# Optimization experiments

Hardware: AMD Instinct MI355X
Metric: run time of the kernel (lower is better)

Reference implementation:

```python
import jax, jax.numpy as jnp
import numpy as np

B, T, E, H = 8, 2048, 512, 16
D = E // H  # 32 embeddings per head
LN_EPS = 1e-3  # keras LayerNormalization default epsilon
DECAY = 1.2


def setup_inputs() -> dict:
    key = jax.random.key(0)
    k0, k1, k2 = jax.random.split(key, 3)
    x = jax.random.normal(k0, (B, T, E), dtype=jnp.float32)
    W = jax.random.normal(k1, (E, E), dtype=jnp.float32) * (1.0 / np.sqrt(E))
    b = jnp.zeros((E,), dtype=jnp.float32)
    concept_map = jax.random.normal(k2, (H, D, D, D), dtype=jnp.float32) * 0.02
    gamma = jnp.ones((E,), dtype=jnp.float32)
    beta = jnp.zeros((E,), dtype=jnp.float32)
    return {"x": x, "W": W, "b": b, "concept_map": concept_map,
            "gamma": gamma, "beta": beta}


def reference(x, W, b, concept_map, gamma, beta):
    Bn, Tn, En = x.shape
    Hn = concept_map.shape[0]
    Dn = En // Hn
    # Dense projection, split into heads: (B,T,H,D)
    h = (jnp.einsum('bte,ef->btf', x, W) + b).reshape(Bn, Tn, Hn, Dn)
    # Decayed cumulative sum of preceding tokens: S_0 = 0, S_t = (S_{t-1} + h_{t-1}) / 1.2
    def step(s, h_t):
        return (s + h_t) / DECAY, s
    _, S = jax.lax.scan(step, jnp.zeros((Bn, Hn, Dn), h.dtype),
                        jnp.swapaxes(h, 0, 1))  # S: (T,B,H,D)
    S = jnp.swapaxes(S, 0, 1)  # (B,T,H,D)
    # Fused bilinear contraction: sum_{i,j} h[...,i] * S[...,j] * C[h,k,i,j]
    # (equivalent to outer-product * concept_map then reduce_sum over last two dims)
    y = jnp.einsum('bthi,bthj,hkij->bthk', h, S, concept_map) + h
    y = y.reshape(Bn, Tn, En)
    # LayerNormalization over last axis (keras default eps=1e-3)
    mu = jnp.mean(y, axis=-1, keepdims=True)
    var = jnp.var(y, axis=-1, keepdims=True)
    y = (y - mu) * jax.lax.rsqrt(var + LN_EPS) * gamma + beta
    # Dropout: identity at inference
    return y
```

## Files before the change

### kernel.cpp

```cpp
#include <hip/hip_runtime.h>
#include <hip/hip_bf16.h>

#define Bn 8
#define Tn 2048
#define En 512
#define Hn 16
#define Dn 32
#define NC 32
#define CL 64
#define NT (Bn*Tn)
#define INV_DECAY (1.0f/1.2f)

typedef __attribute__((ext_vector_type(8))) short  bf16x8;
typedef __attribute__((ext_vector_type(8))) _Float16 f16x8;
typedef __attribute__((ext_vector_type(2))) _Float16 f16x2;
typedef __attribute__((ext_vector_type(4))) float  f32x4;
typedef __attribute__((ext_vector_type(8))) unsigned short u16x8;

__device__ __forceinline__ unsigned short f2b(float f) {
    __hip_bfloat16 h = __float2bfloat16(f);
    return *reinterpret_cast<unsigned short*>(&h);
}
__device__ __forceinline__ float b2f(unsigned short u) {
    union { unsigned int i; float f; } c; c.i = ((unsigned int)u) << 16; return c.f;
}
__device__ __forceinline__ unsigned short f2h(float f) {
    union { _Float16 h; unsigned short u; } c; c.h = (_Float16)f; return c.u;
}

__host__ __device__ constexpr float wpow(int e) {
    float r = 1.f;
    for (int i = 0; i < e; i++) r *= (1.0f / 1.2f);
    return r;
}

__device__ __forceinline__ size_t hm(int hd, int tok, int ch) {
    return (size_t)hd * ((size_t)NT * Dn) + (size_t)tok * Dn + ch;
}

__global__ __launch_bounds__(256) void prep_k(const float* __restrict__ C,
                                              unsigned short* __restrict__ Cl,
                                              const float* __restrict__ W,
                                              unsigned short* __restrict__ Wt) {
    __shared__ float tile[32][33];
    if (blockIdx.x < 256) {
        const int g = blockIdx.x * 256 + threadIdx.x;
        const int hd = g >> 12, rem = g & 4095;
        const int i = rem >> 7, half = (rem >> 6) & 1, lane = rem & 63;
        const int tloc = lane & 15, kgrp = lane >> 4;
        const int k = half * 16 + tloc;
        const float* src = C + (size_t)hd * 32768 + (size_t)k * 1024 + i * 32 + kgrp * 8;
        float4 a = reinterpret_cast<const float4*>(src)[0];
        float4 b = reinterpret_cast<const float4*>(src)[1];
        u16x8 st;
        st[0]=f2h(a.x); st[1]=f2h(a.y); st[2]=f2h(a.z); st[3]=f2h(a.w);
        st[4]=f2h(b.x); st[5]=f2h(b.y); st[6]=f2h(b.z); st[7]=f2h(b.w);
        *reinterpret_cast<u16x8*>(Cl + (size_t)g * 8) = st;
    } else {
        const int bid = blockIdx.x - 256;
        const int kb = (bid & 15) * 32, nb = (bid >> 4) * 32;
        const int tx = threadIdx.x & 31, ty = threadIdx.x >> 5;
        #pragma unroll
        for (int j = 0; j < 4; j++)
            tile[ty + 8 * j][tx] = W[(size_t)(kb + ty + 8 * j) * En + nb + tx];
        __syncthreads();
        #pragma unroll
        for (int j = 0; j < 4; j++)
            Wt[(size_t)(nb + ty + 8 * j) * En + kb + tx] = f2b(tile[tx][ty + 8 * j]);
    }
}

__global__ __launch_bounds__(256) void gemm_mfma_k(const float* __restrict__ x,
                                                   const unsigned short* __restrict__ Wt,
                                                   const float* __restrict__ bias,
                                                   unsigned short* __restrict__ h,
                                                   float* __restrict__ locals) {
    __shared__ unsigned short As[128][40];
    __shared__ unsigned short Bs[64][40];
    const int m0 = blockIdx.x * 128, n0 = blockIdx.y * 64;
    const int tid = threadIdx.x;
    const int wid = tid >> 6, lane = tid & 63;
    const int tloc = lane & 15, kgrp = lane >> 4;
    const int wr = wid >> 1, wc = wid & 1;

    const int ar = tid >> 1, ah = (tid & 1) * 16;
    const int brr = tid >> 2, bq = (tid & 3) * 8;

    f32x4 acc[4][2] = {};

    for (int k0 = 0; k0 < En; k0 += 32) {
        const float* xp = &x[(size_t)(m0 + ar) * En + k0 + ah];
        float4 a0 = reinterpret_cast<const float4*>(xp)[0];
        float4 a1 = reinterpret_cast<const float4*>(xp)[1];
        float4 a2 = reinterpret_cast<const float4*>(xp)[2];
        float4 a3 = reinterpret_cast<const float4*>(xp)[3];
        u16x8 bv = *reinterpret_cast<const u16x8*>(&Wt[(size_t)(n0 + brr) * En + k0 + bq]);
        __syncthreads();
        u16x8 w0, w1;
        w0[0]=f2b(a0.x); w0[1]=f2b(a0.y); w0[2]=f2b(a0.z); w0[3]=f2b(a0.w);
        w0[4]=f2b(a1.x); w0[5]=f2b(a1.y); w0[6]=f2b(a1.z); w0[7]=f2b(a1.w);
        w1[0]=f2b(a2.x); w1[1]=f2b(a2.y); w1[2]=f2b(a2.z); w1[3]=f2b(a2.w);
        w1[4]=f2b(a3.x); w1[5]=f2b(a3.y); w1[6]=f2b(a3.z); w1[7]=f2b(a3.w);
        *reinterpret_cast<u16x8*>(&As[ar][ah])     = w0;
        *reinterpret_cast<u16x8*>(&As[ar][ah + 8]) = w1;
        *reinterpret_cast<u16x8*>(&Bs[brr][bq])    = bv;
        __syncthreads();

        bf16x8 afr[4], bfr[2];
        #pragma unroll
        for (int m = 0; m < 4; m++)
            afr[m] = *reinterpret_cast<const bf16x8*>(&As[wr * 64 + m * 16 + tloc][kgrp * 8]);
        #pragma unroll
        for (int n = 0; n < 2; n++)
            bfr[n] = *reinterpret_cast<const bf16x8*>(&Bs[wc * 32 + n * 16 + tloc][kgrp * 8]);
        #pragma unroll
        for (int m = 0; m < 4; m++)
            #pragma unroll
            for (int n = 0; n < 2; n++)
                acc[m][n] = __builtin_amdgcn_mfma_f32_16x16x32_bf16(afr[m], bfr[n], acc[m][n], 0, 0, 0);
    }

    const float kmul = (kgrp & 1 ? 2.0736f : 1.f) * (kgrp & 2 ? 4.29981696f : 1.f);
    const int cg = blockIdx.x * 2 + wr;

    #pragma unroll
    for (int n = 0; n < 2; n++) {
        const int col = n0 + wc * 32 + n * 16 + tloc;
        const float bcol = bias[col];
        const int hd = col >> 5, ch = col & 31;
        float part = 0.f;
        #pragma unroll
        for (int m = 0; m < 4; m++)
            #pragma unroll
            for (int r = 0; r < 4; r++) {
                const int row = m0 + wr * 64 + m * 16 + kgrp * 4 + r;
                const unsigned short hb16 = f2b(acc[m][n][r] + bcol);
                h[hm(hd, row, ch)] = hb16;
                part += b2f(hb16) * (wpow(64 - m * 16 - r) * kmul);
            }
        part += __shfl_xor(part, 16);
        part += __shfl_xor(part, 32);
        if (kgrp == 0) locals[(size_t)cg * En + col] = part;
    }
}

__global__ __launch_bounds__(512) void scan_emit3_k(const unsigned short* __restrict__ h,
                                                    const float* __restrict__ locals,
                                                    unsigned short* __restrict__ Sg) {
    const int c = blockIdx.x, b = blockIdx.y;
    const int e = threadIdx.x;
    const int hd = e >> 5, ch = e & 31;
    constexpr float INVRL = wpow(64);

    float A = 0.f, w = 1.f;
    for (int cp = c - 1; cp >= 0; --cp) {
        A += w * locals[(size_t)(b * NC + cp) * En + e];
        w *= INVRL;
    }

    const size_t base = hm(hd, b * Tn + c * CL, ch);
    for (int t = 0; t < CL; t++) {
        Sg[base + (size_t)t * Dn] = f2h(A);
        A = (A + b2f(h[base + (size_t)t * Dn])) * INV_DECAY;
    }
}

__global__ __launch_bounds__(256, 4) void bilinear14_k(const unsigned short* __restrict__ hg,
                                                       const unsigned short* __restrict__ Sg,
                                                       unsigned short* __restrict__ yb,
                                                       const unsigned short* __restrict__ Cl) {
    __shared__ float ys[4][64][36];

    const int hd = blockIdx.y;
    const int tid = threadIdx.x;
    const int wid = tid >> 6, lane = tid & 63;
    const int tloc = lane & 15, kgrp = lane >> 4;
    const int j0 = kgrp * 8;
    const int tokens0 = blockIdx.x * 64;

    f16x8 afr[8][2];
    {
        const unsigned short* cb = Cl + (size_t)hd * 32768;
        #pragma unroll
        for (int s = 0; s < 8; s++) {
            const int i = wid * 8 + s;
            #pragma unroll
            for (int mt = 0; mt < 2; mt++)
                afr[s][mt] = *reinterpret_cast<const f16x8*>(
                    cb + ((size_t)((i * 2 + mt) * 64 + lane) * 8));
        }
    }

    _Float16 hh[4][8];
    f16x2 sf2[4][4];
    #pragma unroll
    for (int nt = 0; nt < 4; nt++) {
        const int trow = tokens0 + nt * 16 + tloc;
        u16x8 hv = *reinterpret_cast<const u16x8*>(hg + hm(hd, trow, wid * 8));
        #pragma unroll
        for (int e = 0; e < 8; e++) hh[nt][e] = (_Float16)b2f(hv[e]);
        f16x8 svh = *reinterpret_cast<const f16x8*>(Sg + hm(hd, trow, j0));
        #pragma unroll
        for (int e2 = 0; e2 < 4; e2++) {
            f16x2 p; p.x = svh[e2 * 2]; p.y = svh[e2 * 2 + 1];
            sf2[nt][e2] = p;
        }
    }

    f32x4 acc[2][4] = {};
    #pragma unroll
    for (int s = 0; s < 8; s++) {
        #pragma unroll
        for (int nt = 0; nt < 4; nt++) {
            f16x2 hb; hb.x = hh[nt][s]; hb.y = hh[nt][s];
            union { f16x8 v; f16x2 p[4]; } bf;
            bf.p[0] = sf2[nt][0] * hb;
            bf.p[1] = sf2[nt][1] * hb;
            bf.p[2] = sf2[nt][2] * hb;
            bf.p[3] = sf2[nt][3] * hb;
            acc[0][nt] = __builtin_amdgcn_mfma_f32_16x16x32_f16(afr[s][0], bf.v, acc[0][nt], 0, 0, 0);
            acc[1][nt] = __builtin_amdgcn_mfma_f32_16x16x32_f16(afr[s][1], bf.v, acc[1][nt], 0, 0, 0);
        }
    }

    #pragma unroll
    for (int mt = 0; mt < 2; mt++)
        #pragma unroll
        for (int nt = 0; nt < 4; nt++)
            *reinterpret_cast<f32x4*>(&ys[wid][nt * 16 + tloc][mt * 16 + kgrp * 4]) = acc[mt][nt];
    __syncthreads();

    {
        const int token = tid >> 2, q = tid & 3;
        f32x4 y0 = {0.f,0.f,0.f,0.f}, y1 = {0.f,0.f,0.f,0.f};
        #pragma unroll
        for (int w = 0; w < 4; w++) {
            const f32x4* src = reinterpret_cast<const f32x4*>(&ys[w][token][q * 8]);
            y0 += src[0];
            y1 += src[1];
        }
        u16x8 hres = *reinterpret_cast<const u16x8*>(hg + hm(hd, tokens0 + token, q * 8));
        u16x8 st;
        #pragma unroll
        for (int e = 0; e < 4; e++) {
            st[e]     = f2b(y0[e] + b2f(hres[e]));
            st[4 + e] = f2b(y1[e] + b2f(hres[4 + e]));
        }
        *reinterpret_cast<u16x8*>(yb + hm(hd, tokens0 + token, q * 8)) = st;
    }
}

__global__ __launch_bounds__(256) void ln_k(const unsigned short* __restrict__ y,
                                            const float* __restrict__ gamma,
                                            const float* __restrict__ beta,
                                            float* __restrict__ out) {
    const int row = blockIdx.x * 4 + (threadIdx.x >> 6);
    const int lane = threadIdx.x & 63;
    u16x8 v = *reinterpret_cast<const u16x8*>(y + hm(lane >> 2, row, (lane & 3) * 8));
    float f[8];
    float s = 0.f, s2 = 0.f;
    #pragma unroll
    for (int e = 0; e < 8; e++) {
        f[e] = b2f(v[e]);
        s += f[e]; s2 += f[e] * f[e];
    }
    #pragma unroll
    for (int off = 1; off < 64; off <<= 1) {
        s  += __shfl_xor(s, off);
        s2 += __shfl_xor(s2, off);
    }
    const float mu = s * (1.f / En);
    const float var = s2 * (1.f / En) - mu * mu;
    const float rs = rsqrtf(var + 1e-3f);
    const int cbase = lane * 8;
    float4 g0 = reinterpret_cast<const float4*>(&gamma[cbase])[0];
    float4 g1 = reinterpret_cast<const float4*>(&gamma[cbase])[1];
    float4 b0 = reinterpret_cast<const float4*>(&beta[cbase])[0];
    float4 b1 = reinterpret_cast<const float4*>(&beta[cbase])[1];
    float4 o0, o1;
    o0.x = (f[0] - mu) * rs * g0.x + b0.x; o0.y = (f[1] - mu) * rs * g0.y + b0.y;
    o0.z = (f[2] - mu) * rs * g0.z + b0.z; o0.w = (f[3] - mu) * rs * g0.w + b0.w;
    o1.x = (f[4] - mu) * rs * g1.x + b1.x; o1.y = (f[5] - mu) * rs * g1.y + b1.y;
    o1.z = (f[6] - mu) * rs * g1.z + b1.z; o1.w = (f[7] - mu) * rs * g1.w + b1.w;
    float* op = out + (size_t)row * En;
    reinterpret_cast<float4*>(op)[lane * 2]     = o0;
    reinterpret_cast<float4*>(op)[lane * 2 + 1] = o1;
}

extern "C" void kernel_launch(void* const* d_in, const int* in_sizes, int n_in,
                              void* d_out, int out_size, void* d_ws, size_t ws_size,
                              hipStream_t stream) {
    const float* x     = (const float*)d_in[0];
    const float* W     = (const float*)d_in[1];
    const float* bias  = (const float*)d_in[2];
    const float* C     = (const float*)d_in[3];
    const float* gamma = (const float*)d_in[4];
    const float* beta  = (const float*)d_in[5];
    float* out = (float*)d_out;

    unsigned short* hb  = (unsigned short*)d_ws;
    unsigned short* Sg  = hb + (size_t)Hn * NT * Dn;
    unsigned short* Cl  = Sg + (size_t)Hn * NT * Dn;
    unsigned short* Wt  = Cl + (size_t)Hn * Dn * Dn * Dn;
    float* locals = (float*)(Wt + (size_t)En * En);

    prep_k<<<512, 256, 0, stream>>>(C, Cl, W, Wt);
    gemm_mfma_k<<<dim3(NT / 128, En / 64), 256, 0, stream>>>(x, Wt, bias, hb, locals);
    scan_emit3_k<<<dim3(NC, Bn), 512, 0, stream>>>(hb, locals, Sg);
    bilinear14_k<<<dim3(NT / CL, Hn), 256, 0, stream>>>(hb, Sg, Sg , Cl);
    ln_k<<<NT / 4, 256, 0, stream>>>(Sg, gamma, beta, out);
}
```

Baseline: 76.52 us.

## Switch intermediates from bf16 to fp16 and widen GEMM N-tile to 128

All intermediate tensors (W transpose, projected h, y) now use fp16 instead of bf16, so the GEMM runs fp16 MFMA and the bilinear kernel loads h directly as f16 vectors with no per-element bf16-to-f16 conversion. The projection GEMM tile grows from 128x64 to 128x128, doubling per-warp accumulators and halving the grid, so the x tile is converted and staged in LDS half as often. The costs are fp16 range and overflow risk on h and y, higher register pressure, and fewer blocks available to fill the GPU.

Result: no change. 76.55 us (median of 2 runs) (+0.0%).

```diff
diff --git a/kernel.cpp b/kernel.cpp
--- a/kernel.cpp
+++ b/kernel.cpp
@@ -11,21 +11,16 @@
 #define NT (Bn*Tn)
 #define INV_DECAY (1.0f/1.2f)
 
-typedef __attribute__((ext_vector_type(8))) short  bf16x8;
 typedef __attribute__((ext_vector_type(8))) _Float16 f16x8;
 typedef __attribute__((ext_vector_type(2))) _Float16 f16x2;
 typedef __attribute__((ext_vector_type(4))) float  f32x4;
 typedef __attribute__((ext_vector_type(8))) unsigned short u16x8;
 
-__device__ __forceinline__ unsigned short f2b(float f) {
-    __hip_bfloat16 h = __float2bfloat16(f);
-    return *reinterpret_cast<unsigned short*>(&h);
-}
-__device__ __forceinline__ float b2f(unsigned short u) {
-    union { unsigned int i; float f; } c; c.i = ((unsigned int)u) << 16; return c.f;
-}
 __device__ __forceinline__ unsigned short f2h(float f) {
     union { _Float16 h; unsigned short u; } c; c.h = (_Float16)f; return c.u;
+}
+__device__ __forceinline__ float h2f(unsigned short u) {
+    union { _Float16 h; unsigned short u; } c; c.u = u; return (float)c.h;
 }
 
 __host__ __device__ constexpr float wpow(int e) {
@@ -66,7 +61,7 @@
         __syncthreads();
         #pragma unroll
         for (int j = 0; j < 4; j++)
-            Wt[(size_t)(nb + ty + 8 * j) * En + kb + tx] = f2b(tile[tx][ty + 8 * j]);
+            Wt[(size_t)(nb + ty + 8 * j) * En + kb + tx] = f2h(tile[tx][ty + 8 * j]);
     }
 }
 
@@ -76,56 +71,58 @@
                                                    unsigned short* __restrict__ h,
                                                    float* __restrict__ locals) {
     __shared__ unsigned short As[128][40];
-    __shared__ unsigned short Bs[64][40];
-    const int m0 = blockIdx.x * 128, n0 = blockIdx.y * 64;
+    __shared__ unsigned short Bs[128][40];
+    const int m0 = blockIdx.x * 128, n0 = blockIdx.y * 128;
     const int tid = threadIdx.x;
     const int wid = tid >> 6, lane = tid & 63;
     const int tloc = lane & 15, kgrp = lane >> 4;
     const int wr = wid >> 1, wc = wid & 1;
 
-    const int ar = tid >> 1, ah = (tid & 1) * 16;
-    const int brr = tid >> 2, bq = (tid & 3) * 8;
-
-    f32x4 acc[4][2] = {};
+    const int sr = tid >> 1, sh = (tid & 1) * 16;
+
+    f32x4 acc[4][4] = {};
 
     for (int k0 = 0; k0 < En; k0 += 32) {
-        const float* xp = &x[(size_t)(m0 + ar) * En + k0 + ah];
+        const float* xp = &x[(size_t)(m0 + sr) * En + k0 + sh];
         float4 a0 = reinterpret_cast<const float4*>(xp)[0];
         float4 a1 = reinterpret_cast<const float4*>(xp)[1];
         float4 a2 = reinterpret_cast<const float4*>(xp)[2];
         float4 a3 = reinterpret_cast<const float4*>(xp)[3];
-        u16x8 bv = *reinterpret_cast<const u16x8*>(&Wt[(size_t)(n0 + brr) * En + k0 + bq]);
+        const unsigned short* wp = &Wt[(size_t)(n0 + sr) * En + k0 + sh];
+        u16x8 bv0 = reinterpret_cast<const u16x8*>(wp)[0];
+        u16x8 bv1 = reinterpret_cast<const u16x8*>(wp)[1];
         __syncthreads();
         u16x8 w0, w1;
-        w0[0]=f2b(a0.x); w0[1]=f2b(a0.y); w0[2]=f2b(a0.z); w0[3]=f2b(a0.w);
-        w0[4]=f2b(a1.x); w0[5]=f2b(a1.y); w0[6]=f2b(a1.z); w0[7]=f2b(a1.w);
-        w1[0]=f2b(a2.x); w1[1]=f2b(a2.y); w1[2]=f2b(a2.z); w1[3]=f2b(a2.w);
-        w1[4]=f2b(a3.x); w1[5]=f2b(a3.y); w1[6]=f2b(a3.z); w1[7]=f2b(a3.w);
-        *reinterpret_cast<u16x8*>(&As[ar][ah])     = w0;
-        *reinterpret_cast<u16x8*>(&As[ar][ah + 8]) = w1;
-        *reinterpret_cast<u16x8*>(&Bs[brr][bq])    = bv;
+        w0[0]=f2h(a0.x); w0[1]=f2h(a0.y); w0[2]=f2h(a0.z); w0[3]=f2h(a0.w);
+        w0[4]=f2h(a1.x); w0[5]=f2h(a1.y); w0[6]=f2h(a1.z); w0[7]=f2h(a1.w);
+        w1[0]=f2h(a2.x); w1[1]=f2h(a2.y); w1[2]=f2h(a2.z); w1[3]=f2h(a2.w);
+        w1[4]=f2h(a3.x); w1[5]=f2h(a3.y); w1[6]=f2h(a3.z); w1[7]=f2h(a3.w);
+        *reinterpret_cast<u16x8*>(&As[sr][sh])     = w0;
+        *reinterpret_cast<u16x8*>(&As[sr][sh + 8]) = w1;
+        *reinterpret_cast<u16x8*>(&Bs[sr][sh])     = bv0;
+        *reinterpret_cast<u16x8*>(&Bs[sr][sh + 8]) = bv1;
         __syncthreads();
 
-        bf16x8 afr[4], bfr[2];
+        f16x8 afr[4], bfr[4];
         #pragma unroll
         for (int m = 0; m < 4; m++)
-            afr[m] = *reinterpret_cast<const bf16x8*>(&As[wr * 64 + m * 16 + tloc][kgrp * 8]);
-        #pragma unroll
-        for (int n = 0; n < 2; n++)
-            bfr[n] = *reinterpret_cast<const bf16x8*>(&Bs[wc * 32 + n * 16 + tloc][kgrp * 8]);
+            afr[m] = *reinterpret_cast<const f16x8*>(&As[wr * 64 + m * 16 + tloc][kgrp * 8]);
+        #pragma unroll
+        for (int n = 0; n < 4; n++)
+            bfr[n] = *reinterpret_cast<const f16x8*>(&Bs[wc * 64 + n * 16 + tloc][kgrp * 8]);
         #pragma unroll
         for (int m = 0; m < 4; m++)
             #pragma unroll
-            for (int n = 0; n < 2; n++)
-                acc[m][n] = __builtin_amdgcn_mfma_f32_16x16x32_bf16(afr[m], bfr[n], acc[m][n], 0, 0, 0);
+            for (int n = 0; n < 4; n++)
+                acc[m][n] = __builtin_amdgcn_mfma_f32_16x16x32_f16(afr[m], bfr[n], acc[m][n], 0, 0, 0);
     }
 
     const float kmul = (kgrp & 1 ? 2.0736f : 1.f) * (kgrp & 2 ? 4.29981696f : 1.f);
     const int cg = blockIdx.x * 2 + wr;
 
     #pragma unroll
-    for (int n = 0; n < 2; n++) {
-        const int col = n0 + wc * 32 + n * 16 + tloc;
+    for (int nt = 0; nt < 4; nt++) {
+        const int col = n0 + wc * 64 + nt * 16 + tloc;
         const float bcol = bias[col];
         const int hd = col >> 5, ch = col & 31;
         float part = 0.f;
@@ -134,9 +131,9 @@
             #pragma unroll
             for (int r = 0; r < 4; r++) {
                 const int row = m0 + wr * 64 + m * 16 + kgrp * 4 + r;
-                const unsigned short hb16 = f2b(acc[m][n][r] + bcol);
+                const unsigned short hb16 = f2h(acc[m][nt][r] + bcol);
                 h[hm(hd, row, ch)] = hb16;
-                part += b2f(hb16) * (wpow(64 - m * 16 - r) * kmul);
+                part += h2f(hb16) * (wpow(64 - m * 16 - r) * kmul);
             }
         part += __shfl_xor(part, 16);
         part += __shfl_xor(part, 32);
@@ -161,11 +158,11 @@
     const size_t base = hm(hd, b * Tn + c * CL, ch);
     for (int t = 0; t < CL; t++) {
         Sg[base + (size_t)t * Dn] = f2h(A);
-        A = (A + b2f(h[base + (size_t)t * Dn])) * INV_DECAY;
-    }
-}
-
-__global__ __launch_bounds__(256, 4) void bilinear14_k(const unsigned short* __restrict__ hg,
+        A = (A + h2f(h[base + (size_t)t * Dn])) * INV_DECAY;
+    }
+}
+
+__global__ __launch_bounds__(256, 4) void bilinear15_k(const unsigned short* __restrict__ hg,
                                                        const unsigned short* __restrict__ Sg,
                                                        unsigned short* __restrict__ yb,
                                                        const unsigned short* __restrict__ Cl) {
@@ -191,14 +188,12 @@
         }
     }
 
-    _Float16 hh[4][8];
+    f16x8 hreg[4];
     f16x2 sf2[4][4];
     #pragma unroll
     for (int nt = 0; nt < 4; nt++) {
         const int trow = tokens0 + nt * 16 + tloc;
-        u16x8 hv = *reinterpret_cast<const u16x8*>(hg + hm(hd, trow, wid * 8));
-        #pragma unroll
-        for (int e = 0; e < 8; e++) hh[nt][e] = (_Float16)b2f(hv[e]);
+        hreg[nt] = *reinterpret_cast<const f16x8*>(hg + hm(hd, trow, wid * 8));
         f16x8 svh = *reinterpret_cast<const f16x8*>(Sg + hm(hd, trow, j0));
         #pragma unroll
         for (int e2 = 0; e2 < 4; e2++) {
@@ -212,7 +207,7 @@
     for (int s = 0; s < 8; s++) {
         #pragma unroll
         for (int nt = 0; nt < 4; nt++) {
-            f16x2 hb; hb.x = hh[nt][s]; hb.y = hh[nt][s];
+            f16x2 hb; hb.x = hreg[nt][s]; hb.y = hreg[nt][s];
             union { f16x8 v; f16x2 p[4]; } bf;
             bf.p[0] = sf2[nt][0] * hb;
             bf.p[1] = sf2[nt][1] * hb;
@@ -243,8 +238,8 @@
         u16x8 st;
         #pragma unroll
         for (int e = 0; e < 4; e++) {
-            st[e]     = f2b(y0[e] + b2f(hres[e]));
-            st[4 + e] = f2b(y1[e] + b2f(hres[4 + e]));
+            st[e]     = f2h(y0[e] + h2f(hres[e]));
+            st[4 + e] = f2h(y1[e] + h2f(hres[4 + e]));
         }
         *reinterpret_cast<u16x8*>(yb + hm(hd, tokens0 + token, q * 8)) = st;
     }
@@ -261,7 +256,7 @@
     float s = 0.f, s2 = 0.f;
     #pragma unroll
     for (int e = 0; e < 8; e++) {
-        f[e] = b2f(v[e]);
+        f[e] = h2f(v[e]);
         s += f[e]; s2 += f[e] * f[e];
     }
     #pragma unroll
@@ -305,8 +300,8 @@
     float* locals = (float*)(Wt + (size_t)En * En);
 
     prep_k<<<512, 256, 0, stream>>>(C, Cl, W, Wt);
-    gemm_mfma_k<<<dim3(NT / 128, En / 64), 256, 0, stream>>>(x, Wt, bias, hb, locals);
+    gemm_mfma_k<<<dim3(NT / 128, En / 128), 256, 0, stream>>>(x, Wt, bias, hb, locals);
     scan_emit3_k<<<dim3(NC, Bn), 512, 0, stream>>>(hb, locals, Sg);
-    bilinear14_k<<<dim3(NT / CL, Hn), 256, 0, stream>>>(hb, Sg, Sg , Cl);
+    bilinear15_k<<<dim3(NT / CL, Hn), 256, 0, stream>>>(hb, Sg, Sg , Cl);
     ln_k<<<NT / 4, 256, 0, stream>>>(Sg, gamma, beta, out);
 }
```
